# Optimization experiments

Hardware: AMD Instinct MI355X
Metric: run time of the kernel (lower is better)

Reference implementation:

```python
import jax, jax.numpy as jnp
import numpy as np

N = 6144      # nodes
NFEAT = 512
NHID = 256
NHEADS = 4
DHEAD = NHID // NHEADS  # 64
NEMBED = 128
NEG_INF = -9e15
LRELU_ALPHA = 0.2


def setup_inputs() -> dict:
    key = jax.random.key(0)
    k = jax.random.split(key, 8)
    x = jax.random.normal(k[0], (N, NFEAT), dtype=jnp.float32)
    adj = (jax.random.uniform(k[1], (N, N)) < 0.01).astype(jnp.int32)
    # per-head GAT params, packed over heads
    W = jax.random.normal(k[2], (NHEADS, NFEAT, DHEAD), dtype=jnp.float32) * 0.05
    a_src = jax.random.normal(k[3], (NHEADS, DHEAD), dtype=jnp.float32) * 0.05
    a_dst = jax.random.normal(k[4], (NHEADS, DHEAD), dtype=jnp.float32) * 0.05
    # output linear (init.normal_ std=0.05 per reset_parameters)
    lin_w = jax.random.normal(k[5], (NEMBED, NHID), dtype=jnp.float32) * 0.05
    lin_b = jnp.zeros((NEMBED,), dtype=jnp.float32)
    return {"x": x, "adj": adj, "W": W, "a_src": a_src, "a_dst": a_dst,
            "lin_w": lin_w, "lin_b": lin_b}


def _gat_forward(x, adj, W, a_src, a_dst, lin_w, lin_b):
    # Wh: [H, N, D]
    Wh = jnp.einsum('nf,hfd->hnd', x, W)
    # attention logits e_ij = leakyrelu(a_src.Wh_i + a_dst.Wh_j): [H, N, N]
    s = jnp.einsum('hnd,hd->hn', Wh, a_src)   # source term per node
    t = jnp.einsum('hnd,hd->hn', Wh, a_dst)   # target term per node
    e = s[:, :, None] + t[:, None, :]
    e = jax.nn.leaky_relu(e, negative_slope=LRELU_ALPHA)
    # mask by adjacency, softmax over neighbors
    e = jnp.where(adj[None, :, :] > 0, e, NEG_INF)
    attn = jax.nn.softmax(e, axis=-1)
    # aggregate and per-head ELU (concat=True GAT layer)
    h = jnp.einsum('hnm,hmd->hnd', attn, Wh)
    h = jax.nn.elu(h)
    # concat heads -> [N, NHID]
    h = jnp.transpose(h, (1, 0, 2)).reshape(N, NHID)
    # dropout is identity in eval mode; linear + ELU
    out = jax.nn.elu(h @ lin_w.T + lin_b)
    return out


def reference(x, adj, W, a_src, a_dst, lin_w, lin_b):
    return _gat_forward(x, adj, W, a_src, a_dst, lin_w, lin_b)
```

## Files before the change

### kernel.cpp

```cpp
#include <hip/hip_runtime.h>
#include <hip/hip_bf16.h>
#include <math.h>

#define N_NODES 6144
#define NFEAT 512
#define NHID 256
#define NHEADS 4
#define DHEAD 64
#define NEMBED 128
#define LRELU_ALPHA 0.2f
#define MAXC 256
#define ASTRIDE 20

static __device__ __forceinline__ unsigned short f2bf(float f) {
    unsigned u = __float_as_uint(f);
    unsigned r = (u + 0x7FFFu + ((u >> 16) & 1u)) >> 16;
    return (unsigned short)r;
}
static __device__ __forceinline__ float bfLo(unsigned u) { return __uint_as_float(u << 16); }
static __device__ __forceinline__ float bfHi(unsigned u) { return __uint_as_float(u & 0xffff0000u); }

__global__ __launch_bounds__(256) void gemm_scan(const float* __restrict__ x,
                                                 const float* __restrict__ W,
                                                 const float* __restrict__ a_src,
                                                 const float* __restrict__ a_dst,
                                                 const int* __restrict__ adj,
                                                 unsigned short* __restrict__ Whb,
                                                 float* __restrict__ s_arr,
                                                 float* __restrict__ t_arr,
                                                 int* __restrict__ cnt_g,
                                                 unsigned short* __restrict__ nbr_g) {
    __shared__ float As[64][ASTRIDE];
    __shared__ float Bs[16][64];
    __shared__ int scnt;
    const int tid = threadIdx.x;

    if (blockIdx.y < NHEADS) {
        const int tx = tid & 15;
        const int ty = tid >> 4;
        const int row0 = blockIdx.x * 64;
        const int h = blockIdx.y;
        const float* Bp = W + (size_t)h * NFEAT * DHEAD;

        float acc[4][4] = {};

        for (int k0 = 0; k0 < NFEAT; k0 += 16) {
            {
                const int r = tid >> 2, kq = tid & 3;
                const float4 v = *(const float4*)(x + (size_t)(row0 + r) * NFEAT + k0 + kq * 4);
                *(float4*)&As[r][kq * 4] = v;
            }
            {
                const int kk = tid >> 4, cq = tid & 15;
                const float4 v = *(const float4*)(Bp + (size_t)(k0 + kk) * DHEAD + cq * 4);
                *(float4*)&Bs[kk][cq * 4] = v;
            }
            __syncthreads();
#pragma unroll
            for (int kk = 0; kk < 16; kk++) {
                float a[4], b[4];
#pragma unroll
                for (int i = 0; i < 4; i++) a[i] = As[ty * 4 + i][kk];
#pragma unroll
                for (int j = 0; j < 4; j++) b[j] = Bs[kk][tx * 4 + j];
#pragma unroll
                for (int i = 0; i < 4; i++)
#pragma unroll
                    for (int j = 0; j < 4; j++) acc[i][j] += a[i] * b[j];
            }
            __syncthreads();
        }
#pragma unroll
        for (int i = 0; i < 4; i++) {
            const int row = row0 + ty * 4 + i;
            ushort4 w;
            w.x = f2bf(acc[i][0]);
            w.y = f2bf(acc[i][1]);
            w.z = f2bf(acc[i][2]);
            w.w = f2bf(acc[i][3]);
            *(ushort4*)(Whb + ((size_t)h * N_NODES + row) * DHEAD + tx * 4) = w;
        }
        float a4s[4], a4d[4];
#pragma unroll
        for (int j = 0; j < 4; j++) {
            a4s[j] = a_src[h * DHEAD + tx * 4 + j];
            a4d[j] = a_dst[h * DHEAD + tx * 4 + j];
        }
#pragma unroll
        for (int i = 0; i < 4; i++) {
            float ps = acc[i][0] * a4s[0] + acc[i][1] * a4s[1] +
                       acc[i][2] * a4s[2] + acc[i][3] * a4s[3];
            float pt = acc[i][0] * a4d[0] + acc[i][1] * a4d[1] +
                       acc[i][2] * a4d[2] + acc[i][3] * a4d[3];
#pragma unroll
            for (int off = 1; off < 16; off <<= 1) {
                ps += __shfl_xor(ps, off);
                pt += __shfl_xor(pt, off);
            }
            if (tx == 0) {
                const int row = row0 + ty * 4 + i;
                s_arr[h * N_NODES + row] = ps;
                t_arr[h * N_NODES + row] = pt;
            }
        }
    } else {
        const int r = (blockIdx.y - NHEADS) * gridDim.x + blockIdx.x;
        const int* arow = adj + (size_t)r * N_NODES;
        unsigned short* nrow = nbr_g + (size_t)r * MAXC;
        if (tid == 0) scnt = 0;
        __syncthreads();
#pragma unroll
        for (int it = 0; it < 6; ++it) {
            const int j0 = it * 1024 + tid * 4;
            const int4 v = *(const int4*)(arow + j0);
            const int n = (v.x != 0) + (v.y != 0) + (v.z != 0) + (v.w != 0);
            if (n) {
                int base = atomicAdd(&scnt, n);
                if (v.x) { if (base < MAXC) nrow[base] = (unsigned short)j0; ++base; }
                if (v.y) { if (base < MAXC) nrow[base] = (unsigned short)(j0 + 1); ++base; }
                if (v.z) { if (base < MAXC) nrow[base] = (unsigned short)(j0 + 2); ++base; }
                if (v.w) { if (base < MAXC) nrow[base] = (unsigned short)(j0 + 3); }
            }
        }
        __syncthreads();
        if (tid == 0) cnt_g[r] = scnt;
    }
}

__global__ __launch_bounds__(256) void attn_out(const int* __restrict__ adj,
                                                const unsigned short* __restrict__ Whb,
                                                const float* __restrict__ s_arr,
                                                const float* __restrict__ t_arr,
                                                const int* __restrict__ cnt_g,
                                                const unsigned short* __restrict__ nbr_g,
                                                const float* __restrict__ lin_w,
                                                const float* __restrict__ lin_b,
                                                float* __restrict__ out) {
    __shared__ unsigned short nbr[MAXC];
    __shared__ float p_s[NHEADS][MAXC];
    __shared__ float hrow[NHID];
    __shared__ float part[NEMBED];
    const int i = blockIdx.x;
    const int tid = threadIdx.x;
    const int h = tid >> 6;
    const int lane = tid & 63;
    const int q = lane >> 4;
    const int dq = (lane & 15) * 4;
    const int c = cnt_g[i];
    const unsigned short* wp = Whb + (size_t)h * N_NODES * DHEAD;

    float b0[4] = {0.f, 0.f, 0.f, 0.f};
    float l = 1.0f;
    bool combine = true;

    if (c > 0 && c <= MAXC) {
        for (int k = tid; k < c; k += 256) nbr[k] = nbr_g[(size_t)i * MAXC + k];
        __syncthreads();

        const float s_h = s_arr[h * N_NODES + i];
        const float* tp = t_arr + (size_t)h * N_NODES;
        float m = -INFINITY;
        for (int k = lane; k < c; k += 64) {
            float e = s_h + tp[nbr[k]];
            e = e >= 0.0f ? e : LRELU_ALPHA * e;
            p_s[h][k] = e;
            m = fmaxf(m, e);
        }
#pragma unroll
        for (int off = 32; off > 0; off >>= 1) m = fmaxf(m, __shfl_xor(m, off));
        float ls = 0.0f;
        for (int k = lane; k < c; k += 64) {
            const float p = __expf(p_s[h][k] - m);
            p_s[h][k] = p;
            ls += p;
        }
#pragma unroll
        for (int off = 32; off > 0; off >>= 1) ls += __shfl_xor(ls, off);
        l = ls;

        float b1[4] = {0.f, 0.f, 0.f, 0.f};
        float b2[4] = {0.f, 0.f, 0.f, 0.f};
        float b3[4] = {0.f, 0.f, 0.f, 0.f};
        int k = 0;
        for (; k + 16 <= c; k += 16) {
            const int k0 = k + q, k1 = k + 4 + q, k2 = k + 8 + q, k3 = k + 12 + q;
            const int j0 = nbr[k0], j1 = nbr[k1], j2 = nbr[k2], j3 = nbr[k3];
            const float p0 = p_s[h][k0], p1 = p_s[h][k1];
            const float p2 = p_s[h][k2], p3 = p_s[h][k3];
            const uint2 w0 = *(const uint2*)(wp + (size_t)j0 * DHEAD + dq);
            const uint2 w1 = *(const uint2*)(wp + (size_t)j1 * DHEAD + dq);
            const uint2 w2 = *(const uint2*)(wp + (size_t)j2 * DHEAD + dq);
            const uint2 w3 = *(const uint2*)(wp + (size_t)j3 * DHEAD + dq);
            b0[0] += p0 * bfLo(w0.x); b0[1] += p0 * bfHi(w0.x);
            b0[2] += p0 * bfLo(w0.y); b0[3] += p0 * bfHi(w0.y);
            b1[0] += p1 * bfLo(w1.x); b1[1] += p1 * bfHi(w1.x);
            b1[2] += p1 * bfLo(w1.y); b1[3] += p1 * bfHi(w1.y);
            b2[0] += p2 * bfLo(w2.x); b2[1] += p2 * bfHi(w2.x);
            b2[2] += p2 * bfLo(w2.y); b2[3] += p2 * bfHi(w2.y);
            b3[0] += p3 * bfLo(w3.x); b3[1] += p3 * bfHi(w3.x);
            b3[2] += p3 * bfLo(w3.y); b3[3] += p3 * bfHi(w3.y);
        }
        for (; k < c; k += 4) {
            const int kk = k + q;
            const int j = (kk < c) ? nbr[kk] : nbr[k];
            const float p = (kk < c) ? p_s[h][kk] : 0.0f;
            const uint2 w = *(const uint2*)(wp + (size_t)j * DHEAD + dq);
            b0[0] += p * bfLo(w.x); b0[1] += p * bfHi(w.x);
            b0[2] += p * bfLo(w.y); b0[3] += p * bfHi(w.y);
        }
#pragma unroll
        for (int d = 0; d < 4; d++) b0[d] = (b0[d] + b1[d]) + (b2[d] + b3[d]);
    } else if (c == 0) {
        for (int j = q; j < N_NODES; j += 4) {
            const uint2 w = *(const uint2*)(wp + (size_t)j * DHEAD + dq);
            b0[0] += bfLo(w.x); b0[1] += bfHi(w.x);
            b0[2] += bfLo(w.y); b0[3] += bfHi(w.y);
        }
        l = (float)N_NODES;
    } else {
        combine = false;
        const int* arow = adj + (size_t)i * N_NODES;
        const float s_h = s_arr[h * N_NODES + i];
        const float* tp = t_arr + (size_t)h * N_NODES;
        float m = -INFINITY, ll = 0.0f;
        for (int j = 0; j < N_NODES; j++) {
            if (arow[j]) {
                float e = s_h + tp[j];
                e = e >= 0.0f ? e : LRELU_ALPHA * e;
                const float m_new = fmaxf(m, e);
                const float scale = __expf(m - m_new);
                const float p = __expf(e - m_new);
                ll = ll * scale + p;
                const uint2 w = *(const uint2*)(wp + (size_t)j * DHEAD + dq);
                b0[0] = b0[0] * scale + p * bfLo(w.x);
                b0[1] = b0[1] * scale + p * bfHi(w.x);
                b0[2] = b0[2] * scale + p * bfLo(w.y);
                b0[3] = b0[3] * scale + p * bfHi(w.y);
                m = m_new;
            }
        }
        l = ll;
    }

    if (combine) {
#pragma unroll
        for (int d = 0; d < 4; d++) {
            b0[d] += __shfl_xor(b0[d], 16);
            b0[d] += __shfl_xor(b0[d], 32);
        }
    }
    if (lane < 16) {
        float4 hv;
        float* pv = &hv.x;
#pragma unroll
        for (int d = 0; d < 4; d++) {
            float v = b0[d] / l;
            pv[d] = v > 0.0f ? v : expm1f(v);
        }
        *(float4*)&hrow[h * DHEAD + dq] = hv;
    }
    __syncthreads();

    const float4 hb = *(const float4*)&hrow[lane * 4];
    for (int j = h; j < NEMBED; j += NHEADS) {
        const float4 wv = *(const float4*)(lin_w + (size_t)j * NHID + lane * 4);
        float d = wv.x * hb.x + wv.y * hb.y + wv.z * hb.z + wv.w * hb.w;
#pragma unroll
        for (int off = 32; off > 0; off >>= 1) d += __shfl_xor(d, off);
        if (lane == 0) {
            float val = d + lin_b[j];
            part[j] = val > 0.0f ? val : expm1f(val);
        }
    }
    __syncthreads();
    if (tid < NEMBED) out[(size_t)i * NEMBED + tid] = part[tid];
}

extern "C" void kernel_launch(void* const* d_in, const int* in_sizes, int n_in,
                              void* d_out, int out_size, void* d_ws, size_t ws_size,
                              hipStream_t stream) {
    const float* x     = (const float*)d_in[0];
    const int*   adj   = (const int*)d_in[1];
    const float* W     = (const float*)d_in[2];
    const float* a_src = (const float*)d_in[3];
    const float* a_dst = (const float*)d_in[4];
    const float* lin_w = (const float*)d_in[5];
    const float* lin_b = (const float*)d_in[6];
    float* out = (float*)d_out;

    unsigned short* Whb = (unsigned short*)d_ws;
    float* s    = (float*)(Whb + (size_t)NHEADS * N_NODES * DHEAD);
    float* t    = s + (size_t)NHEADS * N_NODES;
    int* cnt_g  = (int*)(t + (size_t)NHEADS * N_NODES);
    unsigned short* nbr_g = (unsigned short*)(cnt_g + N_NODES);

    gemm_scan<<<dim3(96, NHEADS + 64), 256, 0, stream>>>(
        x, W, a_src, a_dst, adj, Whb, s, t, cnt_g, nbr_g);
    attn_out<<<N_NODES, 256, 0, stream>>>(adj, Whb, s, t, cnt_g, nbr_g,
                                          lin_w, lin_b, out);
}
```

Measured before the change: 322.2 us.

## Split output linear layer into separate tiled GEMM kernel

Moves the final linear+ELU out of the per-node attention kernel into a dedicated shared-memory tiled GEMM over all nodes. The attention kernel now writes concatenated head outputs to a workspace buffer. This avoids every block re-reading the full weight matrix and doing shuffle reductions per output, at the cost of an extra kernel launch and a round trip of the hidden activations through global memory.

```diff
diff --git a/kernel.cpp b/kernel.cpp
--- a/kernel.cpp
+++ b/kernel.cpp
@@ -127,19 +127,15 @@
     }
 }
 
-__global__ __launch_bounds__(256) void attn_out(const int* __restrict__ adj,
+__global__ __launch_bounds__(256) void attn_agg(const int* __restrict__ adj,
                                                 const unsigned short* __restrict__ Whb,
                                                 const float* __restrict__ s_arr,
                                                 const float* __restrict__ t_arr,
                                                 const int* __restrict__ cnt_g,
                                                 const unsigned short* __restrict__ nbr_g,
-                                                const float* __restrict__ lin_w,
-                                                const float* __restrict__ lin_b,
-                                                float* __restrict__ out) {
+                                                float* __restrict__ hcat) {
     __shared__ unsigned short nbr[MAXC];
     __shared__ float p_s[NHEADS][MAXC];
-    __shared__ float hrow[NHID];
-    __shared__ float part[NEMBED];
     const int i = blockIdx.x;
     const int tid = threadIdx.x;
     const int h = tid >> 6;
@@ -257,23 +253,66 @@
             float v = b0[d] / l;
             pv[d] = v > 0.0f ? v : expm1f(v);
         }
-        *(float4*)&hrow[h * DHEAD + dq] = hv;
-    }
-    __syncthreads();
-
-    const float4 hb = *(const float4*)&hrow[lane * 4];
-    for (int j = h; j < NEMBED; j += NHEADS) {
-        const float4 wv = *(const float4*)(lin_w + (size_t)j * NHID + lane * 4);
-        float d = wv.x * hb.x + wv.y * hb.y + wv.z * hb.z + wv.w * hb.w;
-#pragma unroll
-        for (int off = 32; off > 0; off >>= 1) d += __shfl_xor(d, off);
-        if (lane == 0) {
-            float val = d + lin_b[j];
-            part[j] = val > 0.0f ? val : expm1f(val);
-        }
-    }
-    __syncthreads();
-    if (tid < NEMBED) out[(size_t)i * NEMBED + tid] = part[tid];
+        *(float4*)(hcat + (size_t)i * NHID + h * DHEAD + dq) = hv;
+    }
+}
+
+__global__ __launch_bounds__(256) void out_gemm(const float* __restrict__ hcat,
+                                                const float* __restrict__ lin_w,
+                                                const float* __restrict__ lin_b,
+                                                float* __restrict__ out) {
+    __shared__ float As[64][ASTRIDE * 4];
+    __shared__ float Bs[16][64];
+    const int tid = threadIdx.x;
+    const int tx = tid & 15;
+    const int ty = tid >> 4;
+    const int row0 = blockIdx.x * 64;
+    const int c0 = blockIdx.y * 64;
+
+    float acc[4][4] = {};
+
+    for (int k0 = 0; k0 < NHID; k0 += 16) {
+        {
+            const int r = tid >> 2, kq = tid & 3;
+            const float4 v = *(const float4*)(hcat + (size_t)(row0 + r) * NHID + k0 + kq * 4);
+            *(float4*)&As[r][kq * 4] = v;
+        }
+        {
+            const int cc = tid & 63, kq = tid >> 6;
+            const float4 v = *(const float4*)(lin_w + (size_t)(c0 + cc) * NHID + k0 + kq * 4);
+            Bs[kq * 4 + 0][cc] = v.x;
+            Bs[kq * 4 + 1][cc] = v.y;
+            Bs[kq * 4 + 2][cc] = v.z;
+            Bs[kq * 4 + 3][cc] = v.w;
+        }
+        __syncthreads();
+#pragma unroll
+        for (int kk = 0; kk < 16; kk++) {
+            float a[4], b[4];
+#pragma unroll
+            for (int i = 0; i < 4; i++) a[i] = As[ty * 4 + i][kk];
+#pragma unroll
+            for (int j = 0; j < 4; j++) b[j] = Bs[kk][tx * 4 + j];
+#pragma unroll
+            for (int i = 0; i < 4; i++)
+#pragma unroll
+                for (int j = 0; j < 4; j++) acc[i][j] += a[i] * b[j];
+        }
+        __syncthreads();
+    }
+#pragma unroll
+    for (int i = 0; i < 4; i++) {
+        const int row = row0 + ty * 4 + i;
+        float v[4];
+#pragma unroll
+        for (int j = 0; j < 4; j++) {
+            const int col = c0 + tx * 4 + j;
+            float val = acc[i][j] + lin_b[col];
+            v[j] = val > 0.0f ? val : expm1f(val);
+        }
+        *(float4*)(out + (size_t)row * NEMBED + c0 + tx * 4) =
+            make_float4(v[0], v[1], v[2], v[3]);
+    }
 }
 
 extern "C" void kernel_launch(void* const* d_in, const int* in_sizes, int n_in,
@@ -291,11 +330,12 @@
     unsigned short* Whb = (unsigned short*)d_ws;
     float* s    = (float*)(Whb + (size_t)NHEADS * N_NODES * DHEAD);
     float* t    = s + (size_t)NHEADS * N_NODES;
-    int* cnt_g  = (int*)(t + (size_t)NHEADS * N_NODES);
+    float* hcat = t + (size_t)NHEADS * N_NODES;
+    int* cnt_g  = (int*)(hcat + (size_t)N_NODES * NHID);
     unsigned short* nbr_g = (unsigned short*)(cnt_g + N_NODES);
 
     gemm_scan<<<dim3(96, NHEADS + 64), 256, 0, stream>>>(
         x, W, a_src, a_dst, adj, Whb, s, t, cnt_g, nbr_g);
-    attn_out<<<N_NODES, 256, 0, stream>>>(adj, Whb, s, t, cnt_g, nbr_g,
-                                          lin_w, lin_b, out);
-}
+    attn_agg<<<N_NODES, 256, 0, stream>>>(adj, Whb, s, t, cnt_g, nbr_g, hcat);
+    out_gemm<<<dim3(N_NODES / 64, NEMBED / 64), 256, 0, stream>>>(hcat, lin_w, lin_b, out);
+}
```

Result: faster. 278.3 us (-13.6%).
